# Kernel optimization log

Measured on AMD Instinct MI355X. Metric: run time of the kernel, lower is better.

## Reference

```python
import jax, jax.numpy as jnp
import numpy as np

B, N, C, H = 8, 1024, 1024, 16
D = C // H
SCALE = D ** -0.5


def setup_inputs() -> dict:
    key = jax.random.key(0)
    ks = jax.random.split(key, 5)
    s = 0.02  # keep pre-softmax logits in a sane range
    return {
        "x": jax.random.normal(ks[0], (B, N, C), dtype=jnp.float32),
        "Wq": jax.random.normal(ks[1], (C, C), dtype=jnp.float32) * s,
        "bq": jax.random.normal(ks[2], (C,), dtype=jnp.float32) * s,
        "Wkv": jax.random.normal(ks[3], (C, 2 * C), dtype=jnp.float32) * s,
        "bkv": jax.random.normal(ks[4], (2 * C,), dtype=jnp.float32) * s,
    }


def reference(x, Wq, bq, Wkv, bkv):
    b, n, c = x.shape
    h, d = H, c // H
    q = (x @ Wq + bq).reshape(b, n, h, d)                 # [b,n,h,d]
    kv = x @ Wkv + bkv                                     # [b,n,2c]
    k, v = jnp.split(kv, 2, axis=-1)                       # each [b,n,c]
    k = k.reshape(b, n, h, d)
    v = v.reshape(b, n, h, d)
    att = jnp.einsum("bnhd,bmhd->bnmh", q, k) * SCALE      # [b,n,m,h]
    att = jax.nn.softmax(att, axis=2)                      # softmax over keys (m)
    out = jnp.einsum("bnmh,bmhd->bnhd", att, v).reshape(b, n, c)
    return out
```

## Files before the change

### kernel.cpp

```cpp
#include <hip/hip_runtime.h>
#include <stdint.h>

using u16 = unsigned short;
using u32 = unsigned int;
using bf16x8 = __attribute__((ext_vector_type(8))) __bf16;
using f32x4  = __attribute__((ext_vector_type(4))) float;

#define NB 8
#define NN 1024
#define NC 1024
#define NH 16
#define ND 64
#define QSCALE 0.18033688011112042f

__device__ __forceinline__ u16 f2bf(float f) {
  u32 u = __float_as_uint(f);
  return (u16)((u + 0x7fffu + ((u >> 16) & 1u)) >> 16);
}
__device__ __forceinline__ u16 bfc(float f) {
  __bf16 b = (__bf16)f;
  return __builtin_bit_cast(u16, b);
}
__device__ __forceinline__ u32 pack2(u16 a, u16 b) { return (u32)a | ((u32)b << 16); }

__device__ __forceinline__ void gload16(const void* g, void* l) {
  __builtin_amdgcn_global_load_lds((__attribute__((address_space(1))) const u32*)g,
                                   (__attribute__((address_space(3))) u32*)l, 16, 0, 0);
}

__global__ void k_prep(const float* __restrict__ x, const float* __restrict__ Wq,
                       const float* __restrict__ bq, const float* __restrict__ Wkv,
                       const float* __restrict__ bkv,
                       u16* __restrict__ xb, u16* __restrict__ Wt, float* __restrict__ bias) {
  __shared__ u16 tile[64][72];
  int bid = blockIdx.x;
  int t = threadIdx.x;
  if (bid < 8192) {
    int i = bid * 256 + t;
    float4 v = ((const float4*)x)[i];
    ((uint2*)xb)[i] = make_uint2(pack2(f2bf(v.x), f2bf(v.y)), pack2(f2bf(v.z), f2bf(v.w)));
    return;
  }
  if (bid < 8960) {
    int pb = bid - 8192;
    int k0 = (pb & 15) << 6;
    int c0 = (pb >> 4) << 6;
    bool isQ = (c0 < 1024);
    const float* src = isQ ? Wq : Wkv;
    int ldw  = isQ ? 1024 : 2048;
    int csrc = isQ ? c0 : (c0 - 1024);
    float sc = isQ ? QSCALE : 1.0f;

    int r  = t >> 2;
    int cq = (t & 3) << 4;
    const float* p = src + (size_t)(k0 + r) * ldw + csrc + cq;
#pragma unroll
    for (int j = 0; j < 16; j += 4) {
      float4 v = *(const float4*)(p + j);
      tile[r][cq + j + 0] = f2bf(v.x * sc);
      tile[r][cq + j + 1] = f2bf(v.y * sc);
      tile[r][cq + j + 2] = f2bf(v.z * sc);
      tile[r][cq + j + 3] = f2bf(v.w * sc);
    }
    __syncthreads();
    int co = t >> 2;
    int kq = (t & 3) << 4;
    u16 v0[16];
#pragma unroll
    for (int j = 0; j < 16; ++j) v0[j] = tile[kq + j][co];
    uint4 o0, o1;
    o0.x = pack2(v0[0], v0[1]);  o0.y = pack2(v0[2], v0[3]);
    o0.z = pack2(v0[4], v0[5]);  o0.w = pack2(v0[6], v0[7]);
    o1.x = pack2(v0[8], v0[9]);  o1.y = pack2(v0[10], v0[11]);
    o1.z = pack2(v0[12], v0[13]); o1.w = pack2(v0[14], v0[15]);
    u16* dst = Wt + (size_t)(c0 + co) * 1024 + k0 + kq;
    *(uint4*)dst = o0;
    *(uint4*)(dst + 8) = o1;
    return;
  }
  {
    int i = (bid - 8960) * 256 + t;
    if (i < 1024) bias[i] = bq[i] * QSCALE;
    else if (i < 3072) bias[i] = bkv[i - 1024];
  }
}

__launch_bounds__(512, 2)
__global__ void k_gemm(const u16* __restrict__ A, const u16* __restrict__ Bw,
                       const float* __restrict__ bias,
                       u16* __restrict__ qws, u16* __restrict__ kws, u16* __restrict__ vtw) {
  __shared__ __align__(16) u16 LA[2][16384];
  __shared__ __align__(16) u16 LB[2][16384];
  int flat = blockIdx.x;
  int swz = (flat & 7) * 48 + (flat >> 3);
  int m0 = (swz & 31) * 256;
  int n0 = (swz >> 5) * 256;
  int tid = threadIdx.x;
  int w = tid >> 6, lane = tid & 63;
  int lo = lane & 15, hi = lane >> 4;
  int wm = w >> 2, wn = w & 3;

  f32x4 acc[8][4] = {};

  int cs = ((tid & 7) ^ ((tid >> 3) & 7)) * 8;
  const u16* Ag = A  + (size_t)(m0 + (tid >> 3)) * 1024 + cs;
  const u16* Bg = Bw + (size_t)(n0 + (tid >> 3)) * 1024 + cs;

  int ck0 = ((hi ^ (lo & 7)) << 3);
  int ck1 = (((4 + hi) ^ (lo & 7)) << 3);
  const u16* laR = &LA[0][wm * 8192 + lo * 64];
  const u16* lbR = &LB[0][(wn >> 1) * 8192 + ((wn & 1) * 64 + lo) * 64];

#define MFMA_(a, b, c) __builtin_amdgcn_mfma_f32_16x16x32_bf16(a, b, c, 0, 0, 0)
#define SBAR() __builtin_amdgcn_sched_barrier(0); __builtin_amdgcn_s_barrier(); __builtin_amdgcn_sched_barrier(0)
#define LGKM0() asm volatile("s_waitcnt lgkmcnt(0)" ::: "memory"); __builtin_amdgcn_sched_barrier(0)

#define ST_A(BUF, MH, KT)                                                                   \
  gload16(Ag + (size_t)((MH) * 128) * 1024 + (KT) * 64,      &LA[BUF][(MH) * 8192 + tid * 8]); \
  gload16(Ag + (size_t)((MH) * 128 + 64) * 1024 + (KT) * 64, &LA[BUF][(MH) * 8192 + 4096 + tid * 8]);
#define ST_B(BUF, NH, KT)                                                                   \
  gload16(Bg + (size_t)((NH) * 128) * 1024 + (KT) * 64,      &LB[BUF][(NH) * 8192 + tid * 8]); \
  gload16(Bg + (size_t)((NH) * 128 + 64) * 1024 + (KT) * 64, &LB[BUF][(NH) * 8192 + 4096 + tid * 8]);

  ST_A(0, 0, 0); ST_A(0, 1, 0); ST_B(0, 0, 0); ST_B(0, 1, 0);
  ST_A(1, 0, 1); ST_A(1, 1, 1); ST_B(1, 0, 1);
  asm volatile("s_waitcnt vmcnt(6)" ::: "memory");
  __builtin_amdgcn_s_barrier();

#pragma unroll 1
  for (int t = 0; t < 16; ++t) {
    int b = t & 1;
    const u16* la = laR + b * 16384;
    const u16* lb = lbR + b * 16384;
    bf16x8 af[4][2], bf0[2][2], bf1[2][2];

#pragma unroll
    for (int mi = 0; mi < 4; ++mi) {
      af[mi][0] = *(const bf16x8*)(la + mi * 1024 + ck0);
      af[mi][1] = *(const bf16x8*)(la + mi * 1024 + ck1);
    }
#pragma unroll
    for (int ni = 0; ni < 2; ++ni) {
      bf0[ni][0] = *(const bf16x8*)(lb + ni * 1024 + ck0);
      bf0[ni][1] = *(const bf16x8*)(lb + ni * 1024 + ck1);
    }
    if (t < 15) { ST_B(b ^ 1, 1, t + 1); }
    SBAR();
    LGKM0();
    __builtin_amdgcn_s_setprio(1);
#pragma unroll
    for (int ks = 0; ks < 2; ++ks)
#pragma unroll
      for (int mi = 0; mi < 4; ++mi)
#pragma unroll
        for (int ni = 0; ni < 2; ++ni)
          acc[mi][ni] = MFMA_(af[mi][ks], bf0[ni][ks], acc[mi][ni]);
    __builtin_amdgcn_s_setprio(0);
    SBAR();

#pragma unroll
    for (int ni = 0; ni < 2; ++ni) {
      bf1[ni][0] = *(const bf16x8*)(lb + (2 + ni) * 1024 + ck0);
      bf1[ni][1] = *(const bf16x8*)(lb + (2 + ni) * 1024 + ck1);
    }
    SBAR();
    LGKM0();
    __builtin_amdgcn_s_setprio(1);
#pragma unroll
    for (int ks = 0; ks < 2; ++ks)
#pragma unroll
      for (int mi = 0; mi < 4; ++mi)
#pragma unroll
        for (int ni = 0; ni < 2; ++ni)
          acc[mi][2 + ni] = MFMA_(af[mi][ks], bf1[ni][ks], acc[mi][2 + ni]);
    __builtin_amdgcn_s_setprio(0);
    SBAR();

#pragma unroll
    for (int mi = 0; mi < 4; ++mi) {
      af[mi][0] = *(const bf16x8*)(la + (4 + mi) * 1024 + ck0);
      af[mi][1] = *(const bf16x8*)(la + (4 + mi) * 1024 + ck1);
    }
    if (t < 14) { ST_B(b, 0, t + 2); }
    SBAR();
    LGKM0();
    __builtin_amdgcn_s_setprio(1);
#pragma unroll
    for (int ks = 0; ks < 2; ++ks)
#pragma unroll
      for (int mi = 0; mi < 4; ++mi)
#pragma unroll
        for (int ni = 0; ni < 2; ++ni)
          acc[4 + mi][ni] = MFMA_(af[mi][ks], bf0[ni][ks], acc[4 + mi][ni]);
    __builtin_amdgcn_s_setprio(0);
    SBAR();

    if (t < 14) { ST_A(b, 0, t + 2); ST_A(b, 1, t + 2); }
    SBAR();
    __builtin_amdgcn_s_setprio(1);
#pragma unroll
    for (int ks = 0; ks < 2; ++ks)
#pragma unroll
      for (int mi = 0; mi < 4; ++mi)
#pragma unroll
        for (int ni = 0; ni < 2; ++ni)
          acc[4 + mi][2 + ni] = MFMA_(af[mi][ks], bf1[ni][ks], acc[4 + mi][2 + ni]);
    __builtin_amdgcn_s_setprio(0);
    if (t < 14)       { asm volatile("s_waitcnt vmcnt(6)" ::: "memory"); }
    else if (t == 14) { asm volatile("s_waitcnt vmcnt(0)" ::: "memory"); }
    SBAR();
  }
#undef ST_A
#undef ST_B
#undef SBAR
#undef LGKM0
#undef MFMA_

#pragma unroll
  for (int ni = 0; ni < 4; ++ni) {
    int c = n0 + wn * 64 + ni * 16 + lo;
    float bvl = bias[c];
    if (c < 2048) {
#pragma unroll
      for (int mi = 0; mi < 8; ++mi) {
#pragma unroll
        for (int r = 0; r < 4; ++r) {
          int m = m0 + wm * 128 + mi * 16 + hi * 4 + r;
          int b = m >> 10, tok = m & 1023;
          u16 o = f2bf(acc[mi][ni][r] + bvl);
          if (c < 1024) {
            int h = c >> 6, d = c & 63;
            qws[((size_t)(b * 16 + h) * 1024 + tok) * 64 + d] = o;
          } else {
            int c2 = c - 1024; int h = c2 >> 6, d = c2 & 63;
            kws[((size_t)(b * 16 + h) * 1024 + tok) * 64 + d] = o;
          }
        }
      }
    } else {
      int c2 = c - 2048; int h = c2 >> 6, d = c2 & 63;
#pragma unroll
      for (int mi = 0; mi < 8; ++mi) {
        int m = m0 + wm * 128 + mi * 16 + hi * 4;
        int b = m >> 10, tok = m & 1023;
        ushort4 pk;
        pk.x = bfc(acc[mi][ni][0] + bvl);
        pk.y = bfc(acc[mi][ni][1] + bvl);
        pk.z = bfc(acc[mi][ni][2] + bvl);
        pk.w = bfc(acc[mi][ni][3] + bvl);
        *(ushort4*)&vtw[((size_t)(b * 16 + h) * 64 + d) * 1024 + tok] = pk;
      }
    }
  }
}

__launch_bounds__(512)
__global__ void k_attn(const u16* __restrict__ q, const u16* __restrict__ k,
                       const u16* __restrict__ vt, float* __restrict__ out) {
  __shared__ __align__(16) u16 Ks[2][4096];
  __shared__ __align__(16) u16 Vs[2][4096];
  __shared__ __align__(16) u16 P[8][16][72];
  int bh = blockIdx.x;
  int q0 = blockIdx.y * 128;
  int tid = threadIdx.x;
  int w = tid >> 6, lane = tid & 63;
  int lo = lane & 15, hi = lane >> 4;
  int b = bh >> 4, h = bh & 15;

  const u16* kbase = k  + (size_t)bh * 65536;
  const u16* vbase = vt + (size_t)bh * 65536;

  int srow = w * 8 + (lane >> 3);
  int cg   = (lane & 7) ^ ((lane >> 3) & 7);
  const u16* gK = kbase + (size_t)srow * 64   + cg * 8;
  const u16* gV = vbase + (size_t)srow * 1024 + cg * 8;
  u16* lK0 = &Ks[0][w * 512];
  u16* lK1 = &Ks[1][w * 512];
  u16* lV0 = &Vs[0][w * 512];
  u16* lV1 = &Vs[1][w * 512];

  const u16* qp = q + ((size_t)bh * 1024 + q0 + w * 16 + lo) * 64 + hi * 8;
  bf16x8 qf0 = *(const bf16x8*)(qp);
  bf16x8 qf1 = *(const bf16x8*)(qp + 32);

  f32x4 acc_o[4] = {};
  float m_s = -1e30f;
  float l_s = 0.f;

  int sw = lo & 7;

  gload16(gK, lK0);
  gload16(gV, lV0);
  __syncthreads();

  for (int t = 0; t < 16; ++t) {
    int cur = t & 1;
    if (t < 15) {
      gload16(gK + (t + 1) * 4096, cur ? lK0 : lK1);
      gload16(gV + (t + 1) * 64,   cur ? lV0 : lV1);
    }
    f32x4 s[4] = {};
    const u16* kb = Ks[cur];
#pragma unroll
    for (int ni = 0; ni < 4; ++ni) {
      const u16* kp = kb + (ni * 16 + lo) * 64;
      bf16x8 kf0 = *(const bf16x8*)(kp + ((hi ^ sw) * 8));
      bf16x8 kf1 = *(const bf16x8*)(kp + (((4 + hi) ^ sw) * 8));
      s[ni] = __builtin_amdgcn_mfma_f32_16x16x32_bf16(kf0, qf0, s[ni], 0, 0, 0);
      s[ni] = __builtin_amdgcn_mfma_f32_16x16x32_bf16(kf1, qf1, s[ni], 0, 0, 0);
    }
    float pm;
    {
      float a0 = fmaxf(fmaxf(s[0][0], s[0][1]), fmaxf(s[0][2], s[0][3]));
      float a1 = fmaxf(fmaxf(s[1][0], s[1][1]), fmaxf(s[1][2], s[1][3]));
      float a2 = fmaxf(fmaxf(s[2][0], s[2][1]), fmaxf(s[2][2], s[2][3]));
      float a3 = fmaxf(fmaxf(s[3][0], s[3][1]), fmaxf(s[3][2], s[3][3]));
      pm = fmaxf(fmaxf(a0, a1), fmaxf(a2, a3));
      pm = fmaxf(pm, __shfl_xor(pm, 16));
      pm = fmaxf(pm, __shfl_xor(pm, 32));
    }
    if (!__all(pm <= m_s + 8.0f)) {
      float mn = fmaxf(m_s, pm);
      float corr = __builtin_amdgcn_exp2f(m_s - mn);
      m_s = mn;
      l_s *= corr;
      float cr[4];
#pragma unroll
      for (int r = 0; r < 4; ++r) cr[r] = __shfl(corr, hi * 4 + r);
#pragma unroll
      for (int ci = 0; ci < 4; ++ci)
#pragma unroll
        for (int r = 0; r < 4; ++r) acc_o[ci][r] *= cr[r];
    }
    float rs = 0.f;
#pragma unroll
    for (int ni = 0; ni < 4; ++ni) {
      float p0 = __builtin_amdgcn_exp2f(s[ni][0] - m_s);
      float p1 = __builtin_amdgcn_exp2f(s[ni][1] - m_s);
      float p2 = __builtin_amdgcn_exp2f(s[ni][2] - m_s);
      float p3 = __builtin_amdgcn_exp2f(s[ni][3] - m_s);
      rs += (p0 + p1) + (p2 + p3);
      ushort4 pk;
      pk.x = bfc(p0); pk.y = bfc(p1); pk.z = bfc(p2); pk.w = bfc(p3);
      *(ushort4*)&P[w][lo][ni * 16 + hi * 4] = pk;
    }
    rs += __shfl_xor(rs, 16);
    rs += __shfl_xor(rs, 32);
    l_s += rs;
    bf16x8 pf0 = *(const bf16x8*)(&P[w][lo][hi * 8]);
    bf16x8 pf1 = *(const bf16x8*)(&P[w][lo][32 + hi * 8]);
    const u16* vb = Vs[cur];
#pragma unroll
    for (int ci = 0; ci < 4; ++ci) {
      const u16* vp = vb + (ci * 16 + lo) * 64;
      bf16x8 vf0 = *(const bf16x8*)(vp + ((hi ^ sw) * 8));
      bf16x8 vf1 = *(const bf16x8*)(vp + (((4 + hi) ^ sw) * 8));
      acc_o[ci] = __builtin_amdgcn_mfma_f32_16x16x32_bf16(pf0, vf0, acc_o[ci], 0, 0, 0);
      acc_o[ci] = __builtin_amdgcn_mfma_f32_16x16x32_bf16(pf1, vf1, acc_o[ci], 0, 0, 0);
    }
    __syncthreads();
  }
  float inv = 1.0f / l_s;
  float ivr[4];
#pragma unroll
  for (int r = 0; r < 4; ++r) ivr[r] = __shfl(inv, hi * 4 + r);
#pragma unroll
  for (int r = 0; r < 4; ++r) {
    int n = q0 + w * 16 + hi * 4 + r;
    float* dst = out + ((size_t)(b * 1024 + n)) * 1024 + h * 64;
#pragma unroll
    for (int ci = 0; ci < 4; ++ci) dst[ci * 16 + lo] = acc_o[ci][r] * ivr[r];
  }
}

extern "C" void kernel_launch(void* const* d_in, const int* in_sizes, int n_in,
                              void* d_out, int out_size, void* d_ws, size_t ws_size,
                              hipStream_t stream) {
  const float* x   = (const float*)d_in[0];
  const float* Wq  = (const float*)d_in[1];
  const float* bq  = (const float*)d_in[2];
  const float* Wkv = (const float*)d_in[3];
  const float* bkv = (const float*)d_in[4];
  float* out = (float*)d_out;

  char* ws = (char*)d_ws;
  u16*   xb   = (u16*)(ws);
  u16*   Wt   = (u16*)(ws + 16777216);
  float* bias = (float*)(ws + 23068672);
  u16*   qws  = (u16*)(ws + 23080960);
  u16*   kws  = (u16*)(ws + 39858176);
  u16*   vtw  = (u16*)(ws + 73412608);

  k_prep<<<8972, 256, 0, stream>>>(x, Wq, bq, Wkv, bkv, xb, Wt, bias);
  k_gemm<<<384, 512, 0, stream>>>(xb, Wt, bias, qws, kws, vtw);
  {
    dim3 g(128, 8);
    k_attn<<<g, 512, 0, stream>>>(qws, kws, vtw, out);
  }
}
```

Measured before the change: 146.7 us.

## Shrink projection GEMM tile to 256x192 so the grid fills all CUs evenly

Narrows the fused QKV projection GEMM tile from 256x256 to 256x192 and raises the grid from 384 to 512 blocks, so that at two blocks per CU the grid lines up with the 256 CUs instead of leaving a partial second wave. The B tile now streams as three 64-row slabs. The main loop is rescheduled into six MFMA quads, with global-to-LDS loads spread across those phases and the vmcnt waits adjusted. Per-block arithmetic intensity is lower and the A tile is re-read more often, in exchange for better load balance and less LDS use.

After: 138.9 us. 5.3% less time.

```diff
diff --git a/kernel.cpp b/kernel.cpp
--- a/kernel.cpp
+++ b/kernel.cpp
@@ -90,17 +90,17 @@
                        const float* __restrict__ bias,
                        u16* __restrict__ qws, u16* __restrict__ kws, u16* __restrict__ vtw) {
   __shared__ __align__(16) u16 LA[2][16384];
-  __shared__ __align__(16) u16 LB[2][16384];
+  __shared__ __align__(16) u16 LB[2][12288];
   int flat = blockIdx.x;
-  int swz = (flat & 7) * 48 + (flat >> 3);
+  int swz = (flat & 7) * 64 + (flat >> 3);
   int m0 = (swz & 31) * 256;
-  int n0 = (swz >> 5) * 256;
+  int n0 = (swz >> 5) * 192;
   int tid = threadIdx.x;
   int w = tid >> 6, lane = tid & 63;
   int lo = lane & 15, hi = lane >> 4;
   int wm = w >> 2, wn = w & 3;
 
-  f32x4 acc[8][4] = {};
+  f32x4 acc[8][3] = {};
 
   int cs = ((tid & 7) ^ ((tid >> 3) & 7)) * 8;
   const u16* Ag = A  + (size_t)(m0 + (tid >> 3)) * 1024 + cs;
@@ -109,71 +109,64 @@
   int ck0 = ((hi ^ (lo & 7)) << 3);
   int ck1 = (((4 + hi) ^ (lo & 7)) << 3);
   const u16* laR = &LA[0][wm * 8192 + lo * 64];
-  const u16* lbR = &LB[0][(wn >> 1) * 8192 + ((wn & 1) * 64 + lo) * 64];
+  const u16* lbR = &LB[0][(wn * 48 + lo) * 64];
 
 #define MFMA_(a, b, c) __builtin_amdgcn_mfma_f32_16x16x32_bf16(a, b, c, 0, 0, 0)
 #define SBAR() __builtin_amdgcn_sched_barrier(0); __builtin_amdgcn_s_barrier(); __builtin_amdgcn_sched_barrier(0)
 #define LGKM0() asm volatile("s_waitcnt lgkmcnt(0)" ::: "memory"); __builtin_amdgcn_sched_barrier(0)
 
-#define ST_A(BUF, MH, KT)                                                                   \
+#define ST_AH(BUF, MH, KT)                                                                     \
   gload16(Ag + (size_t)((MH) * 128) * 1024 + (KT) * 64,      &LA[BUF][(MH) * 8192 + tid * 8]); \
   gload16(Ag + (size_t)((MH) * 128 + 64) * 1024 + (KT) * 64, &LA[BUF][(MH) * 8192 + 4096 + tid * 8]);
-#define ST_B(BUF, NH, KT)                                                                   \
-  gload16(Bg + (size_t)((NH) * 128) * 1024 + (KT) * 64,      &LB[BUF][(NH) * 8192 + tid * 8]); \
-  gload16(Bg + (size_t)((NH) * 128 + 64) * 1024 + (KT) * 64, &LB[BUF][(NH) * 8192 + 4096 + tid * 8]);
-
-  ST_A(0, 0, 0); ST_A(0, 1, 0); ST_B(0, 0, 0); ST_B(0, 1, 0);
-  ST_A(1, 0, 1); ST_A(1, 1, 1); ST_B(1, 0, 1);
-  asm volatile("s_waitcnt vmcnt(6)" ::: "memory");
+#define ST_BT(BUF, NH, KT)                                                                     \
+  gload16(Bg + (size_t)((NH) * 64) * 1024 + (KT) * 64,       &LB[BUF][(NH) * 4096 + tid * 8]);
+
+#define QUAD(Q, NI)                                                           \
+  __builtin_amdgcn_s_setprio(1);                                              \
+  _Pragma("unroll")                                                           \
+  for (int ks = 0; ks < 2; ++ks)                                              \
+    _Pragma("unroll")                                                         \
+    for (int mi = 0; mi < 4; ++mi)                                            \
+      acc[(Q) * 4 + mi][NI] = MFMA_(af[mi][ks], bfr[NI][ks], acc[(Q) * 4 + mi][NI]); \
+  __builtin_amdgcn_s_setprio(0);
+
+  ST_AH(0, 0, 0); ST_AH(0, 1, 0); ST_BT(0, 0, 0); ST_BT(0, 1, 0); ST_BT(0, 2, 0);
+  ST_AH(1, 0, 1); ST_AH(1, 1, 1); ST_BT(1, 0, 1); ST_BT(1, 1, 1); ST_BT(1, 2, 1);
+  asm volatile("s_waitcnt vmcnt(7)" ::: "memory");
   __builtin_amdgcn_s_barrier();
 
 #pragma unroll 1
   for (int t = 0; t < 16; ++t) {
     int b = t & 1;
     const u16* la = laR + b * 16384;
-    const u16* lb = lbR + b * 16384;
-    bf16x8 af[4][2], bf0[2][2], bf1[2][2];
+    const u16* lb = lbR + b * 12288;
+    bf16x8 af[4][2], bfr[3][2];
+    bool st = (t < 14);
 
 #pragma unroll
     for (int mi = 0; mi < 4; ++mi) {
       af[mi][0] = *(const bf16x8*)(la + mi * 1024 + ck0);
       af[mi][1] = *(const bf16x8*)(la + mi * 1024 + ck1);
     }
-#pragma unroll
-    for (int ni = 0; ni < 2; ++ni) {
-      bf0[ni][0] = *(const bf16x8*)(lb + ni * 1024 + ck0);
-      bf0[ni][1] = *(const bf16x8*)(lb + ni * 1024 + ck1);
-    }
-    if (t < 15) { ST_B(b ^ 1, 1, t + 1); }
+    bfr[0][0] = *(const bf16x8*)(lb + ck0);
+    bfr[0][1] = *(const bf16x8*)(lb + ck1);
     SBAR();
     LGKM0();
-    __builtin_amdgcn_s_setprio(1);
-#pragma unroll
-    for (int ks = 0; ks < 2; ++ks)
-#pragma unroll
-      for (int mi = 0; mi < 4; ++mi)
-#pragma unroll
-        for (int ni = 0; ni < 2; ++ni)
-          acc[mi][ni] = MFMA_(af[mi][ks], bf0[ni][ks], acc[mi][ni]);
-    __builtin_amdgcn_s_setprio(0);
-    SBAR();
-
-#pragma unroll
-    for (int ni = 0; ni < 2; ++ni) {
-      bf1[ni][0] = *(const bf16x8*)(lb + (2 + ni) * 1024 + ck0);
-      bf1[ni][1] = *(const bf16x8*)(lb + (2 + ni) * 1024 + ck1);
-    }
+    QUAD(0, 0);
+    SBAR();
+
+    bfr[1][0] = *(const bf16x8*)(lb + 1024 + ck0);
+    bfr[1][1] = *(const bf16x8*)(lb + 1024 + ck1);
     SBAR();
     LGKM0();
-    __builtin_amdgcn_s_setprio(1);
-#pragma unroll
-    for (int ks = 0; ks < 2; ++ks)
-#pragma unroll
-      for (int mi = 0; mi < 4; ++mi)
-#pragma unroll
-        for (int ni = 0; ni < 2; ++ni)
-          acc[mi][2 + ni] = MFMA_(af[mi][ks], bf1[ni][ks], acc[mi][2 + ni]);
-    __builtin_amdgcn_s_setprio(0);
+    QUAD(0, 1);
+    SBAR();
+
+    bfr[2][0] = *(const bf16x8*)(lb + 2048 + ck0);
+    bfr[2][1] = *(const bf16x8*)(lb + 2048 + ck1);
+    SBAR();
+    LGKM0();
+    QUAD(0, 2);
     SBAR();
 
 #pragma unroll
@@ -181,44 +174,34 @@
       af[mi][0] = *(const bf16x8*)(la + (4 + mi) * 1024 + ck0);
       af[mi][1] = *(const bf16x8*)(la + (4 + mi) * 1024 + ck1);
     }
-    if (t < 14) { ST_B(b, 0, t + 2); }
+    if (st) { ST_BT(b, 0, t + 2); }
     SBAR();
     LGKM0();
-    __builtin_amdgcn_s_setprio(1);
-#pragma unroll
-    for (int ks = 0; ks < 2; ++ks)
-#pragma unroll
-      for (int mi = 0; mi < 4; ++mi)
-#pragma unroll
-        for (int ni = 0; ni < 2; ++ni)
-          acc[4 + mi][ni] = MFMA_(af[mi][ks], bf0[ni][ks], acc[4 + mi][ni]);
-    __builtin_amdgcn_s_setprio(0);
-    SBAR();
-
-    if (t < 14) { ST_A(b, 0, t + 2); ST_A(b, 1, t + 2); }
-    SBAR();
-    __builtin_amdgcn_s_setprio(1);
-#pragma unroll
-    for (int ks = 0; ks < 2; ++ks)
-#pragma unroll
-      for (int mi = 0; mi < 4; ++mi)
-#pragma unroll
-        for (int ni = 0; ni < 2; ++ni)
-          acc[4 + mi][2 + ni] = MFMA_(af[mi][ks], bf1[ni][ks], acc[4 + mi][2 + ni]);
-    __builtin_amdgcn_s_setprio(0);
-    if (t < 14)       { asm volatile("s_waitcnt vmcnt(6)" ::: "memory"); }
+    QUAD(1, 0);
+    SBAR();
+
+    if (st) { ST_AH(b, 0, t + 2); ST_BT(b, 1, t + 2); }
+    SBAR();
+    QUAD(1, 1);
+    SBAR();
+
+    if (st) { ST_AH(b, 1, t + 2); ST_BT(b, 2, t + 2); }
+    SBAR();
+    QUAD(1, 2);
+    if (t < 14)       { asm volatile("s_waitcnt vmcnt(7)" ::: "memory"); }
     else if (t == 14) { asm volatile("s_waitcnt vmcnt(0)" ::: "memory"); }
     SBAR();
   }
-#undef ST_A
-#undef ST_B
+#undef QUAD
+#undef ST_AH
+#undef ST_BT
 #undef SBAR
 #undef LGKM0
 #undef MFMA_
 
 #pragma unroll
-  for (int ni = 0; ni < 4; ++ni) {
-    int c = n0 + wn * 64 + ni * 16 + lo;
+  for (int ni = 0; ni < 3; ++ni) {
+    int c = n0 + wn * 48 + ni * 16 + lo;
     float bvl = bias[c];
     if (c < 2048) {
 #pragma unroll
@@ -392,7 +375,7 @@
   u16*   vtw  = (u16*)(ws + 73412608);
 
   k_prep<<<8972, 256, 0, stream>>>(x, Wq, bq, Wkv, bkv, xb, Wt, bias);
-  k_gemm<<<384, 512, 0, stream>>>(xb, Wt, bias, qws, kws, vtw);
+  k_gemm<<<512, 512, 0, stream>>>(xb, Wt, bias, qws, kws, vtw);
   {
     dim3 g(128, 8);
     k_attn<<<g, 512, 0, stream>>>(qws, kws, vtw, out);
```
